# Optimization experiments

Measured on AMD Instinct MI355X. Metric: run time of the kernel, lower is better.

Reference implementation:

```python
import jax, jax.numpy as jnp
import numpy as np

B = 256          # number of graphs
D = 256          # hidden_dim
H = 4            # num_heads
S = 4            # num_seeds
DH = D // H      # head dim = 64
MAX_NODES = 2048 # max nodes per graph (padding target)


def setup_inputs() -> dict:
    key = jax.random.key(0)
    ks = jax.random.split(key, 8)
    # per-graph node counts, constructed so they sum exactly to B*1024 = 262144
    rng = np.random.RandomState(0)
    delta = rng.randint(0, 960, size=B // 2)
    counts = np.concatenate([1024 + delta, 1024 - delta]).astype(np.int32)
    N = int(counts.sum())  # 262144
    return {
        "node_feat": jax.random.normal(ks[0], (N, D), dtype=jnp.float32),
        "batch_num_nodes": jnp.asarray(counts),
        "seeds": jax.random.normal(ks[1], (S, D), dtype=jnp.float32),
        "in_proj_w": jax.random.normal(ks[2], (3 * D, D), dtype=jnp.float32) * 0.02,
        "in_proj_b": jnp.zeros((3 * D,), jnp.float32),
        "out_proj_w": jax.random.normal(ks[3], (D, D), dtype=jnp.float32) * 0.02,
        "out_proj_b": jnp.zeros((D,), jnp.float32),
        "fc1_w": jax.random.normal(ks[4], (D, S * D), dtype=jnp.float32) * 0.02,
        "fc1_b": jnp.zeros((D,), jnp.float32),
        "fc2_w": jax.random.normal(ks[5], (D, D), dtype=jnp.float32) * 0.02,
        "fc2_b": jnp.zeros((D,), jnp.float32),
    }


def reference(node_feat, batch_num_nodes, seeds, in_proj_w, in_proj_b,
              out_proj_w, out_proj_b, fc1_w, fc1_b, fc2_w, fc2_b):
    N = node_feat.shape[0]
    counts = batch_num_nodes
    # ragged -> padded [B, MAX_NODES, D] via scatter (equiv. of split + zero-pad + stack)
    offsets = jnp.concatenate([jnp.zeros((1,), counts.dtype), jnp.cumsum(counts)[:-1]])
    gid = jnp.repeat(jnp.arange(B, dtype=counts.dtype), counts, total_repeat_length=N)
    pos = jnp.arange(N, dtype=counts.dtype) - offsets[gid]
    padded = jnp.zeros((B, MAX_NODES, D), node_feat.dtype).at[gid, pos].set(node_feat)
    pad_mask = jnp.arange(MAX_NODES)[None, :] >= counts[:, None]  # True = padding key

    # torch nn.MultiheadAttention: packed in_proj split into q/k/v
    Wq, Wk, Wv = jnp.split(in_proj_w, 3, axis=0)
    bq, bk, bv = jnp.split(in_proj_b, 3)
    q = (seeds @ Wq.T + bq).reshape(S, H, DH)                 # [S,H,DH] (broadcast over B)
    k = (padded @ Wk.T + bk).reshape(B, MAX_NODES, H, DH)     # [B,M,H,DH]
    v = (padded @ Wv.T + bv).reshape(B, MAX_NODES, H, DH)

    scale = 1.0 / jnp.sqrt(jnp.asarray(DH, q.dtype))
    scores = jnp.einsum('shd,bmhd->bhsm', q, k) * scale       # [B,H,S,M]
    scores = jnp.where(pad_mask[:, None, None, :], jnp.asarray(-1e9, scores.dtype), scores)
    attn = jax.nn.softmax(scores, axis=-1)
    ctx = jnp.einsum('bhsm,bmhd->bshd', attn, v).reshape(B, S, D)
    attended = ctx @ out_proj_w.T + out_proj_b                # [B,S,D]

    # output_proj: Linear(S*D, D) -> GELU(exact) -> Linear(D, D)
    flat = attended.reshape(B, S * D)
    h = jax.nn.gelu(flat @ fc1_w.T + fc1_b, approximate=False)
    return h @ fc2_w.T + fc2_b                                # [B,D]
```

## Files before the change

kernel.cpp:

```cpp
#include <hip/hip_runtime.h>

#define D 256
#define SH 16
#define Ss 4
#define CH 256
#define NT 64
#define XS_STRIDE 272
#define WB_STRIDE 80

typedef _Float16 half8 __attribute__((ext_vector_type(8)));
typedef _Float16 half4 __attribute__((ext_vector_type(4)));
typedef float f32x4 __attribute__((ext_vector_type(4)));

#define OFF_AF16   ((size_t)0)
#define OFF_CM     ((size_t)8192)
#define OFF_Q      ((size_t)8448)
#define OFF_DESC   ((size_t)12544)
#define OFF_SUMEXP ((size_t)33280)
#define OFF_ACC    ((size_t)49664)
#define OFF_WVT    ((size_t)4243968)
#define OFF_WOT    ((size_t)4506112)
#define OFF_FC1T   ((size_t)4768256)
#define OFF_FC2T   ((size_t)5816832)

__global__ void k_prep(const float* __restrict__ seeds,
                       const float* __restrict__ inw,
                       const float* __restrict__ inb,
                       const int* __restrict__ counts,
                       char* __restrict__ ws) {
  int t = threadIdx.x;
  if (blockIdx.x < 4) {
    int s = blockIdx.x;
    __shared__ float sv[D];
    sv[t] = seeds[s * D + t];
    __syncthreads();
    const float4* wr = (const float4*)(inw + (size_t)t * D);
    float acc = inb[t];
    #pragma unroll 8
    for (int j = 0; j < 64; j++) {
      float4 w4 = wr[j];
      acc += w4.x * sv[4*j] + w4.y * sv[4*j+1] + w4.z * sv[4*j+2] + w4.w * sv[4*j+3];
    }
    ((float*)(ws + OFF_Q))[s * D + t] = acc;
  } else {
    __shared__ int s1[256], s2[256];
    int cnt = counts[t];
    int nch = (cnt + CH - 1) / CH;
    s1[t] = cnt; s2[t] = nch;
    __syncthreads();
    for (int off = 1; off < 256; off <<= 1) {
      int a1 = (t >= off) ? s1[t - off] : 0;
      int a2 = (t >= off) ? s2[t - off] : 0;
      __syncthreads();
      s1[t] += a1; s2[t] += a2;
      __syncthreads();
    }
    int start = s1[t] - cnt, cb = s2[t] - nch;
    int4* desc = (int4*)(ws + OFF_DESC + 16);
    for (int j = 0; j < nch; j++) {
      int nn = cnt - j * CH; if (nn > CH) nn = CH;
      desc[cb + j] = make_int4(t, start + j * CH, nn, 0);
    }
    if (t == 255) *(int*)(ws + OFF_DESC) = s2[255];
  }
}

__global__ void k_mk_a(const float* __restrict__ inw, char* __restrict__ ws) {
  int sh = blockIdx.x;
  int s = sh >> 2, h = sh & 3;
  int j = threadIdx.x;
  __shared__ float qh[64];
  __shared__ float red[256];
  if (j < 64) qh[j] = ((const float*)(ws + OFF_Q))[s * D + h * 64 + j];
  __syncthreads();
  const float* wk = inw + (size_t)(D + h * 64) * D;
  float a = 0.f;
  #pragma unroll 8
  for (int d = 0; d < 64; d++) a += qh[d] * wk[(size_t)d * D + j];
  a *= 0.125f;
  ((_Float16*)(ws + OFF_AF16))[sh * D + j] = (_Float16)a;
  red[j] = a * a;
  __syncthreads();
  for (int st = 128; st > 0; st >>= 1) { if (j < st) red[j] += red[j + st]; __syncthreads(); }
  if (j == 0) ((float*)(ws + OFF_CM))[sh] = -6.0f * sqrtf(red[0]);
}

__global__ void k_transpose(const float* __restrict__ inw, const float* __restrict__ ow,
                            const float* __restrict__ f1w, const float* __restrict__ f2w,
                            char* __restrict__ ws) {
  int b = blockIdx.x;
  const float* src; float* dst; int R, C, ti, tj;
  if (b < 64)       { src = inw + (size_t)512 * D; dst = (float*)(ws + OFF_WVT);  R = 256; C = 256;  int x = b;        tj = x / 8;  ti = x % 8; }
  else if (b < 128) { src = ow;                    dst = (float*)(ws + OFF_WOT);  R = 256; C = 256;  int x = b - 64;   tj = x / 8;  ti = x % 8; }
  else if (b < 192) { src = f2w;                   dst = (float*)(ws + OFF_FC2T); R = 256; C = 256;  int x = b - 128;  tj = x / 8;  ti = x % 8; }
  else              { src = f1w;                   dst = (float*)(ws + OFF_FC1T); R = 256; C = 1024; int x = b - 192;  tj = x / 8;  ti = x % 8; }
  __shared__ float tl[32][33];
  int tx = threadIdx.x & 31, ty = threadIdx.x >> 5;
  #pragma unroll
  for (int k = 0; k < 4; k++) {
    int r = ty + k * 8;
    tl[r][tx] = src[(size_t)(ti * 32 + r) * C + tj * 32 + tx];
  }
  __syncthreads();
  #pragma unroll
  for (int k = 0; k < 4; k++) {
    int r = ty + k * 8;
    dst[(size_t)(tj * 32 + r) * R + ti * 32 + tx] = tl[tx][r];
  }
}

__launch_bounds__(256, 4)
__global__ void k_main(const float* __restrict__ nf, char* __restrict__ ws) {
  int nchunks = *(const int*)(ws + OFF_DESC);
  if ((int)blockIdx.x >= nchunks) return;
  int4 dsc = ((const int4*)(ws + OFF_DESC + 16))[blockIdx.x];
  int g = dsc.x, start = dsc.y, cnt = dsc.z;

  __shared__ _Float16 xs[NT * XS_STRIDE];
  __shared__ _Float16 wb[SH * WB_STRIDE];

  int t = threadIdx.x;
  int lane = t & 63, wv = t >> 6;
  int col = lane & 15, q = lane >> 4;

  const _Float16* af = (const _Float16*)(ws + OFF_AF16);
  half8 aw[8];
  #pragma unroll
  for (int kc = 0; kc < 8; kc++) aw[kc] = *(const half8*)(af + col * D + kc * 32 + q * 8);
  float cmv = ((const float*)(ws + OFF_CM))[col];

  f32x4 acc[4] = {{0,0,0,0},{0,0,0,0},{0,0,0,0},{0,0,0,0}};
  float dsum = 0.f;

  int ntile = (cnt + NT - 1) / NT;
  for (int tile = 0; tile < ntile; tile++) {
    #pragma unroll 4
    for (int p = 0; p < 16; p++) {
      int flat = p * 256 + t;
      int row = flat >> 6, c4 = flat & 63;
      int nloc = tile * NT + row;
      float4 v = make_float4(0.f, 0.f, 0.f, 0.f);
      if (nloc < cnt) v = ((const float4*)(nf + (size_t)(start + nloc) * D))[c4];
      half4 hv;
      hv[0] = (_Float16)v.x; hv[1] = (_Float16)v.y; hv[2] = (_Float16)v.z; hv[3] = (_Float16)v.w;
      *(half4*)(xs + row * XS_STRIDE + c4 * 4) = hv;
    }
    __syncthreads();

    f32x4 sc = {0, 0, 0, 0};
    const _Float16* xrow = xs + (wv * 16 + col) * XS_STRIDE + q * 8;
    #pragma unroll
    for (int kc = 0; kc < 8; kc++) {
      half8 xa = *(const half8*)(xrow + kc * 32);
      sc = __builtin_amdgcn_mfma_f32_16x16x32_f16(xa, aw[kc], sc, 0, 0, 0);
    }
    #pragma unroll
    for (int r = 0; r < 4; r++) {
      int nloc = wv * 16 + q * 4 + r;
      float arg = fminf(sc[r] + cmv, 10.f);
      float wj = (tile * NT + nloc < cnt) ? __expf(arg) : 0.f;
      _Float16 wh = (_Float16)wj;
      dsum += (float)wh;
      wb[col * WB_STRIDE + nloc] = wh;
    }
    __syncthreads();

    #pragma unroll
    for (int ks = 0; ks < 2; ks++) {
      half8 wa = *(const half8*)(wb + col * WB_STRIDE + ks * 32 + q * 8);
      #pragma unroll
      for (int dt = 0; dt < 4; dt++) {
        int dd = wv * 64 + dt * 16 + col;
        half8 xb;
        #pragma unroll
        for (int jj = 0; jj < 8; jj++) xb[jj] = xs[(ks * 32 + q * 8 + jj) * XS_STRIDE + dd];
        acc[dt] = __builtin_amdgcn_mfma_f32_16x16x32_f16(wa, xb, acc[dt], 0, 0, 0);
      }
    }
    __syncthreads();
  }

  dsum += __shfl_xor(dsum, 16);
  dsum += __shfl_xor(dsum, 32);
  if (q == 0) atomicAdd(((float*)(ws + OFF_SUMEXP)) + g * SH + col, dsum);
  float* accw = (float*)(ws + OFF_ACC);
  #pragma unroll
  for (int dt = 0; dt < 4; dt++)
    #pragma unroll
    for (int r = 0; r < 4; r++)
      atomicAdd(&accw[(size_t)(g * SH + q * 4 + r) * D + wv * 64 + dt * 16 + col], acc[dt][r]);
}

__global__ void k_final(const float* __restrict__ inb, const float* __restrict__ ob,
                        const float* __restrict__ f1b, const float* __restrict__ f2b,
                        const char* __restrict__ ws, float* __restrict__ out) {
  int t = threadIdx.x;
  int g0 = blockIdx.x * 2;
  const float* sume = (const float*)(ws + OFF_SUMEXP);
  const float* accw = (const float*)(ws + OFF_ACC);
  const float* WvT = (const float*)(ws + OFF_WVT);
  const float* WoT = (const float*)(ws + OFF_WOT);
  const float* F1T = (const float*)(ws + OFF_FC1T);
  const float* F2T = (const float*)(ws + OFF_FC2T);

  __shared__ float xb2[2][SH][D];
  __shared__ float cx2[2][Ss][D];
  __shared__ float fl2[2][1024];
  __shared__ float hh2[2][D];
  __shared__ float inv[32];

  if (t < 32) inv[t] = 1.0f / sume[(g0 + (t >> 4)) * SH + (t & 15)];
  __syncthreads();
  for (int e = t; e < 2 * SH * D; e += 256) {
    int gg = e >> 12, sh = (e >> 8) & 15, d = e & 255;
    xb2[gg][sh][d] = accw[(size_t)(g0 + gg) * SH * D + sh * D + d] * inv[gg * 16 + sh];
  }
  __syncthreads();

  {
    float ca[2][4] = {{0,0,0,0},{0,0,0,0}};
    int h = t >> 6;
    for (int d = 0; d < D; d++) {
      float wvd = WvT[(size_t)d * D + t];
      #pragma unroll
      for (int gg = 0; gg < 2; gg++)
        #pragma unroll
        for (int s = 0; s < 4; s++)
          ca[gg][s] += wvd * xb2[gg][s * 4 + h][d];
    }
    float bv = inb[2 * D + t];
    #pragma unroll
    for (int gg = 0; gg < 2; gg++)
      #pragma unroll
      for (int s = 0; s < 4; s++) cx2[gg][s][t] = ca[gg][s] + bv;
  }
  __syncthreads();
  {
    float aa[2][4] = {{0,0,0,0},{0,0,0,0}};
    for (int d = 0; d < D; d++) {
      float wod = WoT[(size_t)d * D + t];
      #pragma unroll
      for (int gg = 0; gg < 2; gg++)
        #pragma unroll
        for (int s = 0; s < 4; s++)
          aa[gg][s] += wod * cx2[gg][s][d];
    }
    float bo = ob[t];
    #pragma unroll
    for (int gg = 0; gg < 2; gg++)
      #pragma unroll
      for (int s = 0; s < 4; s++) fl2[gg][s * D + t] = aa[gg][s] + bo;
  }
  __syncthreads();
  {
    float f1[2] = {0, 0};
    for (int k = 0; k < 1024; k++) {
      float w1 = F1T[(size_t)k * D + t];
      f1[0] += w1 * fl2[0][k];
      f1[1] += w1 * fl2[1][k];
    }
    #pragma unroll
    for (int gg = 0; gg < 2; gg++) {
      float x = f1[gg] + f1b[t];
      hh2[gg][t] = 0.5f * x * (1.0f + erff(x * 0.70710678118654752f));
    }
  }
  __syncthreads();
  {
    float f2[2] = {0, 0};
    for (int d = 0; d < D; d++) {
      float w2 = F2T[(size_t)d * D + t];
      f2[0] += w2 * hh2[0][d];
      f2[1] += w2 * hh2[1][d];
    }
    #pragma unroll
    for (int gg = 0; gg < 2; gg++) out[(size_t)(g0 + gg) * D + t] = f2[gg] + f2b[t];
  }
}

extern "C" void kernel_launch(void* const* d_in, const int* in_sizes, int n_in,
                              void* d_out, int out_size, void* d_ws, size_t ws_size,
                              hipStream_t stream) {
  const float* nf    = (const float*)d_in[0];
  const int*   cnts  = (const int*)d_in[1];
  const float* seeds = (const float*)d_in[2];
  const float* inw   = (const float*)d_in[3];
  const float* inb   = (const float*)d_in[4];
  const float* ow    = (const float*)d_in[5];
  const float* obv   = (const float*)d_in[6];
  const float* f1w   = (const float*)d_in[7];
  const float* f1b   = (const float*)d_in[8];
  const float* f2w   = (const float*)d_in[9];
  const float* f2b   = (const float*)d_in[10];
  char* ws = (char*)d_ws;
  float* out = (float*)d_out;
  int N = in_sizes[0] / D;

  hipMemsetAsync(ws + OFF_SUMEXP, 0, (size_t)16384 + 4194304, stream);
  k_prep<<<5, 256, 0, stream>>>(seeds, inw, inb, cnts, ws);
  k_mk_a<<<16, 256, 0, stream>>>(inw, ws);
  k_transpose<<<448, 256, 0, stream>>>(inw, ow, f1w, f2w, ws);
  int maxc = (N + CH - 1) / CH + 256;
  k_main<<<maxc, 256, 0, stream>>>(nf, ws);
  k_final<<<128, 256, 0, stream>>>(inb, obv, f1b, f2b, ws, out);
}
```

Measured before the change: 547.7 us.

## Replace atomics with per-chunk partials and merge setup kernels into one launch

The main kernel now writes each chunk's partial accumulator and exp-sum to a dedicated workspace slot instead of using global atomicAdds. The final kernel reduces those partials per graph using a chunk prefix table. This removes the memset and the atomic contention. The three setup kernels (q/A computation, chunk descriptors, weight transposes) are fused into a single launch to cut launch overhead. The trade-off is a larger workspace and extra partial-buffer traffic read in the final kernel. The load loop unroll is also raised.

```diff
diff --git a/kernel.cpp b/kernel.cpp
--- a/kernel.cpp
+++ b/kernel.cpp
@@ -2,47 +2,65 @@
 
 #define D 256
 #define SH 16
-#define Ss 4
 #define CH 256
 #define NT 64
 #define XS_STRIDE 272
 #define WB_STRIDE 80
+#define PSTRIDE (17*256)
 
 typedef _Float16 half8 __attribute__((ext_vector_type(8)));
 typedef _Float16 half4 __attribute__((ext_vector_type(4)));
 typedef float f32x4 __attribute__((ext_vector_type(4)));
 
-#define OFF_AF16   ((size_t)0)
-#define OFF_CM     ((size_t)8192)
-#define OFF_Q      ((size_t)8448)
-#define OFF_DESC   ((size_t)12544)
-#define OFF_SUMEXP ((size_t)33280)
-#define OFF_ACC    ((size_t)49664)
-#define OFF_WVT    ((size_t)4243968)
-#define OFF_WOT    ((size_t)4506112)
-#define OFF_FC1T   ((size_t)4768256)
-#define OFF_FC2T   ((size_t)5816832)
-
-__global__ void k_prep(const float* __restrict__ seeds,
-                       const float* __restrict__ inw,
-                       const float* __restrict__ inb,
-                       const int* __restrict__ counts,
-                       char* __restrict__ ws) {
+#define OFF_AF16 ((size_t)0)
+#define OFF_CM   ((size_t)8192)
+#define OFF_GC   ((size_t)8448)
+#define OFF_DESC ((size_t)9728)
+#define OFF_PART ((size_t)31744)
+#define OFF_WVT  ((size_t)23428096)
+#define OFF_WOT  (OFF_WVT + 262144)
+#define OFF_FC1T (OFF_WOT + 262144)
+#define OFF_FC2T (OFF_FC1T + 1048576)
+
+__global__ void k_setup(const float* __restrict__ seeds,
+                        const float* __restrict__ inw,
+                        const float* __restrict__ inb,
+                        const int* __restrict__ counts,
+                        const float* __restrict__ ow,
+                        const float* __restrict__ f1w,
+                        const float* __restrict__ f2w,
+                        char* __restrict__ ws) {
   int t = threadIdx.x;
-  if (blockIdx.x < 4) {
-    int s = blockIdx.x;
+  int b = blockIdx.x;
+  if (b < 16) {
+    int s = b >> 2, h = b & 3;
     __shared__ float sv[D];
+    __shared__ float qh[64];
+    __shared__ float red[256];
     sv[t] = seeds[s * D + t];
     __syncthreads();
-    const float4* wr = (const float4*)(inw + (size_t)t * D);
-    float acc = inb[t];
+    if (t < 64) {
+      const float4* wr = (const float4*)(inw + (size_t)(h * 64 + t) * D);
+      float acc = inb[h * 64 + t];
+      #pragma unroll 8
+      for (int j = 0; j < 64; j++) {
+        float4 w4 = wr[j];
+        acc += w4.x * sv[4*j] + w4.y * sv[4*j+1] + w4.z * sv[4*j+2] + w4.w * sv[4*j+3];
+      }
+      qh[t] = acc;
+    }
+    __syncthreads();
+    const float* wk = inw + (size_t)(D + h * 64) * D;
+    float a = 0.f;
     #pragma unroll 8
-    for (int j = 0; j < 64; j++) {
-      float4 w4 = wr[j];
-      acc += w4.x * sv[4*j] + w4.y * sv[4*j+1] + w4.z * sv[4*j+2] + w4.w * sv[4*j+3];
-    }
-    ((float*)(ws + OFF_Q))[s * D + t] = acc;
-  } else {
+    for (int d = 0; d < 64; d++) a += qh[d] * wk[(size_t)d * D + t];
+    a *= 0.125f;
+    ((_Float16*)(ws + OFF_AF16))[b * D + t] = (_Float16)a;
+    red[t] = a * a;
+    __syncthreads();
+    for (int st = 128; st > 0; st >>= 1) { if (t < st) red[t] += red[t + st]; __syncthreads(); }
+    if (t == 0) ((float*)(ws + OFF_CM))[b] = -6.0f * sqrtf(red[0]);
+  } else if (b == 16) {
     __shared__ int s1[256], s2[256];
     int cnt = counts[t];
     int nch = (cnt + CH - 1) / CH;
@@ -56,65 +74,43 @@
       __syncthreads();
     }
     int start = s1[t] - cnt, cb = s2[t] - nch;
-    int4* desc = (int4*)(ws + OFF_DESC + 16);
+    int* gc = (int*)(ws + OFF_GC);
+    gc[t + 1] = s2[t];
+    if (t == 0) gc[0] = 0;
+    int4* desc = (int4*)(ws + OFF_DESC);
     for (int j = 0; j < nch; j++) {
       int nn = cnt - j * CH; if (nn > CH) nn = CH;
       desc[cb + j] = make_int4(t, start + j * CH, nn, 0);
     }
-    if (t == 255) *(int*)(ws + OFF_DESC) = s2[255];
-  }
-}
-
-__global__ void k_mk_a(const float* __restrict__ inw, char* __restrict__ ws) {
-  int sh = blockIdx.x;
-  int s = sh >> 2, h = sh & 3;
-  int j = threadIdx.x;
-  __shared__ float qh[64];
-  __shared__ float red[256];
-  if (j < 64) qh[j] = ((const float*)(ws + OFF_Q))[s * D + h * 64 + j];
-  __syncthreads();
-  const float* wk = inw + (size_t)(D + h * 64) * D;
-  float a = 0.f;
-  #pragma unroll 8
-  for (int d = 0; d < 64; d++) a += qh[d] * wk[(size_t)d * D + j];
-  a *= 0.125f;
-  ((_Float16*)(ws + OFF_AF16))[sh * D + j] = (_Float16)a;
-  red[j] = a * a;
-  __syncthreads();
-  for (int st = 128; st > 0; st >>= 1) { if (j < st) red[j] += red[j + st]; __syncthreads(); }
-  if (j == 0) ((float*)(ws + OFF_CM))[sh] = -6.0f * sqrtf(red[0]);
-}
-
-__global__ void k_transpose(const float* __restrict__ inw, const float* __restrict__ ow,
-                            const float* __restrict__ f1w, const float* __restrict__ f2w,
-                            char* __restrict__ ws) {
-  int b = blockIdx.x;
-  const float* src; float* dst; int R, C, ti, tj;
-  if (b < 64)       { src = inw + (size_t)512 * D; dst = (float*)(ws + OFF_WVT);  R = 256; C = 256;  int x = b;        tj = x / 8;  ti = x % 8; }
-  else if (b < 128) { src = ow;                    dst = (float*)(ws + OFF_WOT);  R = 256; C = 256;  int x = b - 64;   tj = x / 8;  ti = x % 8; }
-  else if (b < 192) { src = f2w;                   dst = (float*)(ws + OFF_FC2T); R = 256; C = 256;  int x = b - 128;  tj = x / 8;  ti = x % 8; }
-  else              { src = f1w;                   dst = (float*)(ws + OFF_FC1T); R = 256; C = 1024; int x = b - 192;  tj = x / 8;  ti = x % 8; }
-  __shared__ float tl[32][33];
-  int tx = threadIdx.x & 31, ty = threadIdx.x >> 5;
-  #pragma unroll
-  for (int k = 0; k < 4; k++) {
-    int r = ty + k * 8;
-    tl[r][tx] = src[(size_t)(ti * 32 + r) * C + tj * 32 + tx];
-  }
-  __syncthreads();
-  #pragma unroll
-  for (int k = 0; k < 4; k++) {
-    int r = ty + k * 8;
-    dst[(size_t)(tj * 32 + r) * R + ti * 32 + tx] = tl[tx][r];
+  } else {
+    int x = b - 17;
+    const float* src; float* dst; int R, C, ti, tj;
+    if (x < 64)       { src = inw + (size_t)512 * D; dst = (float*)(ws + OFF_WVT);  R = 256; C = 256;  tj = x / 8;        ti = x % 8; }
+    else if (x < 128) { src = ow;                    dst = (float*)(ws + OFF_WOT);  R = 256; C = 256;  tj = (x-64) / 8;   ti = x % 8; }
+    else if (x < 192) { src = f2w;                   dst = (float*)(ws + OFF_FC2T); R = 256; C = 256;  tj = (x-128) / 8;  ti = x % 8; }
+    else              { src = f1w;                   dst = (float*)(ws + OFF_FC1T); R = 256; C = 1024; tj = (x-192) / 8;  ti = x % 8; }
+    __shared__ float tl[32][33];
+    int tx = t & 31, ty = t >> 5;
+    #pragma unroll
+    for (int k = 0; k < 4; k++) {
+      int r = ty + k * 8;
+      tl[r][tx] = src[(size_t)(ti * 32 + r) * C + tj * 32 + tx];
+    }
+    __syncthreads();
+    #pragma unroll
+    for (int k = 0; k < 4; k++) {
+      int r = ty + k * 8;
+      dst[(size_t)(tj * 32 + r) * R + ti * 32 + tx] = tl[tx][r];
+    }
   }
 }
 
 __launch_bounds__(256, 4)
 __global__ void k_main(const float* __restrict__ nf, char* __restrict__ ws) {
-  int nchunks = *(const int*)(ws + OFF_DESC);
+  int nchunks = ((const int*)(ws + OFF_GC))[256];
   if ((int)blockIdx.x >= nchunks) return;
-  int4 dsc = ((const int4*)(ws + OFF_DESC + 16))[blockIdx.x];
-  int g = dsc.x, start = dsc.y, cnt = dsc.z;
+  int4 dsc = ((const int4*)(ws + OFF_DESC))[blockIdx.x];
+  int start = dsc.y, cnt = dsc.z;
 
   __shared__ _Float16 xs[NT * XS_STRIDE];
   __shared__ _Float16 wb[SH * WB_STRIDE];
@@ -134,7 +130,7 @@
 
   int ntile = (cnt + NT - 1) / NT;
   for (int tile = 0; tile < ntile; tile++) {
-    #pragma unroll 4
+    #pragma unroll 8
     for (int p = 0; p < 16; p++) {
       int flat = p * 256 + t;
       int row = flat >> 6, c4 = flat & 63;
@@ -182,13 +178,13 @@
 
   dsum += __shfl_xor(dsum, 16);
   dsum += __shfl_xor(dsum, 32);
-  if (q == 0) atomicAdd(((float*)(ws + OFF_SUMEXP)) + g * SH + col, dsum);
-  float* accw = (float*)(ws + OFF_ACC);
+  float* pp = (float*)(ws + OFF_PART) + (size_t)blockIdx.x * PSTRIDE;
   #pragma unroll
   for (int dt = 0; dt < 4; dt++)
     #pragma unroll
     for (int r = 0; r < 4; r++)
-      atomicAdd(&accw[(size_t)(g * SH + q * 4 + r) * D + wv * 64 + dt * 16 + col], acc[dt][r]);
+      pp[(q * 4 + r) * D + wv * 64 + dt * 16 + col] = acc[dt][r];
+  if (q == 0) pp[16 * D + wv * 64 + col] = dsum;
 }
 
 __global__ void k_final(const float* __restrict__ inb, const float* __restrict__ ob,
@@ -196,24 +192,34 @@
                         const char* __restrict__ ws, float* __restrict__ out) {
   int t = threadIdx.x;
   int g0 = blockIdx.x * 2;
-  const float* sume = (const float*)(ws + OFF_SUMEXP);
-  const float* accw = (const float*)(ws + OFF_ACC);
+  const int* gc = (const int*)(ws + OFF_GC);
+  const float* part = (const float*)(ws + OFF_PART);
   const float* WvT = (const float*)(ws + OFF_WVT);
   const float* WoT = (const float*)(ws + OFF_WOT);
   const float* F1T = (const float*)(ws + OFF_FC1T);
   const float* F2T = (const float*)(ws + OFF_FC2T);
 
   __shared__ float xb2[2][SH][D];
-  __shared__ float cx2[2][Ss][D];
+  __shared__ float cx2[2][4][D];
   __shared__ float fl2[2][1024];
   __shared__ float hh2[2][D];
   __shared__ float inv[32];
 
-  if (t < 32) inv[t] = 1.0f / sume[(g0 + (t >> 4)) * SH + (t & 15)];
+  if (t < 32) {
+    int gg = t >> 4, col = t & 15, g = g0 + gg;
+    float s = 0.f;
+    for (int c = gc[g]; c < gc[g + 1]; c++)
+      for (int wv = 0; wv < 4; wv++)
+        s += part[(size_t)c * PSTRIDE + 16 * D + wv * 64 + col];
+    inv[t] = 1.0f / s;
+  }
   __syncthreads();
   for (int e = t; e < 2 * SH * D; e += 256) {
-    int gg = e >> 12, sh = (e >> 8) & 15, d = e & 255;
-    xb2[gg][sh][d] = accw[(size_t)(g0 + gg) * SH * D + sh * D + d] * inv[gg * 16 + sh];
+    int gg = e >> 12, row = (e >> 8) & 15, d = e & 255, g = g0 + gg;
+    float s = 0.f;
+    for (int c = gc[g]; c < gc[g + 1]; c++)
+      s += part[(size_t)c * PSTRIDE + row * D + d];
+    xb2[gg][row][d] = s * inv[gg * 16 + row];
   }
   __syncthreads();
 
@@ -296,10 +302,7 @@
   float* out = (float*)d_out;
   int N = in_sizes[0] / D;
 
-  hipMemsetAsync(ws + OFF_SUMEXP, 0, (size_t)16384 + 4194304, stream);
-  k_prep<<<5, 256, 0, stream>>>(seeds, inw, inb, cnts, ws);
-  k_mk_a<<<16, 256, 0, stream>>>(inw, ws);
-  k_transpose<<<448, 256, 0, stream>>>(inw, ow, f1w, f2w, ws);
+  k_setup<<<465, 256, 0, stream>>>(seeds, inw, inb, cnts, ow, f1w, f2w, ws);
   int maxc = (N + CH - 1) / CH + 256;
   k_main<<<maxc, 256, 0, stream>>>(nf, ws);
   k_final<<<128, 256, 0, stream>>>(inb, obv, f1b, f2b, ws, out);
```

Result: no change. 557.9 us (+1.9%).
